# Optimization experiments

Measured on AMD Instinct MI355X. Metric: run time of the kernel, lower is better.

Reference implementation:

```python
import jax, jax.numpy as jnp
import numpy as np

B, S, D, H = 2, 2048, 1024, 16
DH = D // H


def setup_inputs() -> dict:
    key = jax.random.key(0)
    ks = jax.random.split(key, 9)
    s = 0.02
    return {
        "x": jax.random.normal(ks[0], (B, S, D), dtype=jnp.float32),
        "Wq": jax.random.normal(ks[1], (D, D), dtype=jnp.float32) * s,
        "bq": jnp.zeros((D,), dtype=jnp.float32),
        "Wk": jax.random.normal(ks[2], (D, D), dtype=jnp.float32) * s,
        "bk": jnp.zeros((D,), dtype=jnp.float32),
        "Wv": jax.random.normal(ks[3], (D, D), dtype=jnp.float32) * s,
        "bv": jnp.zeros((D,), dtype=jnp.float32),
        "Wo": jax.random.normal(ks[4], (D, D), dtype=jnp.float32) * s,
        "bo": jnp.zeros((D,), dtype=jnp.float32),
    }


def _split_heads(t):
    # [B,S,D] -> [B,H,S,Dh]
    return t.reshape(B, S, H, DH).transpose(0, 2, 1, 3)


def reference(x, Wq, bq, Wk, bk, Wv, bv, Wo, bo):
    q = _split_heads(x @ Wq + bq)
    k = _split_heads(x @ Wk + bk)
    v = _split_heads(x @ Wv + bv)
    scale = 1.0 / jnp.sqrt(jnp.float32(DH))
    # [B,H,S,S] attention scores (naive, materialized as in original)
    scores = jnp.einsum("bhqd,bhkd->bhqk", q, k) * scale
    probs = jax.nn.softmax(scores, axis=-1)
    attn = jnp.einsum("bhqk,bhkd->bhqd", probs, v)
    out = attn.transpose(0, 2, 1, 3).reshape(B, S, D)
    return out @ Wo + bo
```

## Files before the change

kernel.cpp:

```cpp
#include <hip/hip_runtime.h>
#include <math.h>

#define NB 2
#define NS 2048
#define ND 1024
#define NH 16
#define NDH 64
#define NM (NB * NS)
#define K2 (2 * ND)

typedef unsigned short ushortT;
typedef __attribute__((ext_vector_type(8))) short bf16x8;
typedef __attribute__((ext_vector_type(4))) float f32x4;
typedef __attribute__((ext_vector_type(16))) float f32x16;

__device__ inline unsigned short f2bf(float f) {
    union { float f; unsigned u; } v; v.f = f;
    unsigned r = v.u + 0x7FFFu + ((v.u >> 16) & 1u);
    return (unsigned short)(r >> 16);
}
__device__ inline float bf2f(unsigned short h) {
    union { unsigned u; float f; } v; v.u = ((unsigned)h) << 16; return v.f;
}
__device__ inline unsigned cvt_pk_bf16(float lo, float hi) {
    unsigned r;
    asm("v_cvt_pk_bf16_f32 %0, %1, %2" : "=v"(r) : "v"(lo), "v"(hi));
    return r;
}
__device__ inline void gl_lds16(const ushortT* g, ushortT* l) {
    __builtin_amdgcn_global_load_lds(
        (const __attribute__((address_space(1))) unsigned*)g,
        (__attribute__((address_space(3))) unsigned*)l, 16, 0, 0);
}

#define QSC 0.18033688011112042f

__global__ __launch_bounds__(256) void split_x(
    const float* __restrict__ x, ushortT* __restrict__ xh)
{
    int idx = (blockIdx.x * 256 + threadIdx.x) * 4;
    float4 v = *(const float4*)&x[idx];
    float fv[4] = {v.x, v.y, v.z, v.w};
    union { ushortT s[4]; uint2 u; } o;
#pragma unroll
    for (int j = 0; j < 4; ++j) o.s[j] = f2bf(fv[j]);
    *(uint2*)&xh[idx] = o.u;
}

__global__ __launch_bounds__(256) void split_w_t(
    const float* __restrict__ Wq, const float* __restrict__ Wk,
    const float* __restrict__ Wv, const float* __restrict__ Wo,
    ushortT* __restrict__ WtH, ushortT* __restrict__ WtO)
{
    const int z = blockIdx.z;
    const float* __restrict__ W = (z == 0) ? Wq : (z == 1) ? Wk : (z == 2) ? Wv : Wo;

    const int k0 = blockIdx.y * 64, n0 = blockIdx.x * 64;
    const int t = threadIdx.x;
    __shared__ float Ls[64][65];

#pragma unroll
    for (int i = 0; i < 4; ++i) {
        int kl = i * 16 + (t >> 4);
        int nl = (t & 15) << 2;
        float4 w4 = *(const float4*)&W[(size_t)(k0 + kl) * ND + n0 + nl];
        Ls[nl + 0][kl] = w4.x;
        Ls[nl + 1][kl] = w4.y;
        Ls[nl + 2][kl] = w4.z;
        Ls[nl + 3][kl] = w4.w;
    }
    __syncthreads();
#pragma unroll
    for (int i = 0; i < 16; ++i) {
        int flat = i * 256 + t;
        int n = flat >> 6, kk = flat & 63;
        float val = Ls[n][kk];
        unsigned short hi = f2bf(val);
        if (z < 3) {
            WtH[(size_t)z * ND * ND + (size_t)(n0 + n) * ND + (k0 + kk)] = hi;
        } else {
            WtO[(size_t)(n0 + n) * K2 + (k0 + kk)]      = hi;
            WtO[(size_t)(n0 + n) * K2 + ND + (k0 + kk)] = f2bf(val - bf2f(hi));
        }
    }
}

template <int OUTMODE>
__global__ __launch_bounds__(256) void gemm_split(
    const ushortT* __restrict__ A2,
    const ushortT* __restrict__ Wt,
    const float* __restrict__ b0, const float* __restrict__ b1, const float* __restrict__ b2,
    ushortT* __restrict__ Qo, ushortT* __restrict__ Ko, ushortT* __restrict__ Vtg,
    float* __restrict__ Ofp)
{
    const int z = blockIdx.z;
    const int AS = OUTMODE ? K2 : ND;
    const ushortT* __restrict__ Bt = OUTMODE ? Wt : Wt + (size_t)z * ND * ND;
    const float* __restrict__ bias = (z == 0) ? b0 : (z == 1) ? b1 : b2;

    const int L = blockIdx.y * 8 + blockIdx.x;
    const int rx = L & 7, q = L >> 3;
    const int m0 = (((q >> 3) << 3) + rx) * 128;
    const int n0 = (q & 7) * 128;

    const int tid = threadIdx.x;
    const int lane = tid & 63, w = tid >> 6;
    const int wrow = w >> 1, wcol = w & 1;
    const int a = lane & 15, g = lane >> 4;

    __shared__ __align__(16) ushortT Abuf[3][128 * 32];
    __shared__ __align__(16) ushortT Bbuf[3][128 * 32];

    f32x4 acc[4][4] = {};

    const int srow_l = tid >> 2;
    const int scc0 = tid & 3;
    const int swz = (a >> 1) & 3;

    const int nst = OUTMODE ? 96 : 32;

    auto stage = [&](int bufi, int ks) {
        const int kp = ks * 32;
        const int ac = OUTMODE ? ((kp < ND) ? kp : kp - ND) : kp;
        const int bc = OUTMODE ? ((kp < 2 * ND) ? kp : kp - 2 * ND) : kp;
#pragma unroll
        for (int t = 0; t < 2; ++t) {
            int r = t * 64 + srow_l;
            int sc = scc0 ^ ((r >> 1) & 3);
            gl_lds16(&A2[(size_t)(m0 + r) * AS + ac + (sc << 3)],
                     &Abuf[bufi][(t * 256 + w * 64) * 8]);
            gl_lds16(&Bt[(size_t)(n0 + r) * AS + bc + (sc << 3)],
                     &Bbuf[bufi][(t * 256 + w * 64) * 8]);
        }
    };

    stage(0, 0);
    stage(1, 1);
    int cur = 0;
    for (int i = 0; i < nst; ++i) {
        if (i + 1 < nst) {
            asm volatile("s_waitcnt vmcnt(4)" ::: "memory");
        } else {
            asm volatile("s_waitcnt vmcnt(0)" ::: "memory");
        }
        __builtin_amdgcn_s_barrier();

        if (i + 2 < nst) {
            int nb = cur + 2; if (nb >= 3) nb -= 3;
            stage(nb, i + 2);
        }

        bf16x8 af[4], bfr[4];
#pragma unroll
        for (int ii = 0; ii < 4; ++ii)
            af[ii] = *(const bf16x8*)&Abuf[cur][(wrow * 64 + ii * 16 + a) * 32 + ((g ^ swz) << 3)];
#pragma unroll
        for (int j = 0; j < 4; ++j)
            bfr[j] = *(const bf16x8*)&Bbuf[cur][(wcol * 64 + j * 16 + a) * 32 + ((g ^ swz) << 3)];
#pragma unroll
        for (int ii = 0; ii < 4; ++ii)
#pragma unroll
            for (int j = 0; j < 4; ++j)
                acc[ii][j] = __builtin_amdgcn_mfma_f32_16x16x32_bf16(af[ii], bfr[j], acc[ii][j], 0, 0, 0);

        ++cur; if (cur == 3) cur = 0;
    }

    float bj[4];
#pragma unroll
    for (int j = 0; j < 4; ++j) bj[j] = bias[n0 + wcol * 64 + j * 16 + a];

#pragma unroll
    for (int i = 0; i < 4; ++i) {
#pragma unroll
        for (int r = 0; r < 4; ++r) {
            int grow = m0 + wrow * 64 + i * 16 + g * 4 + r;
#pragma unroll
            for (int j = 0; j < 4; ++j) {
                int gcol = n0 + wcol * 64 + j * 16 + a;
                float v = acc[i][j][r] + bj[j];
                if (OUTMODE == 1) {
                    Ofp[(size_t)grow * ND + gcol] = v;
                } else {
                    int b = grow >> 11, s = grow & (NS - 1);
                    int h = gcol >> 6, dh = gcol & 63;
                    if (z == 0) {
                        Qo[((size_t)(b * NH + h) * NS + s) * NDH + dh] = f2bf(v * QSC);
                    } else if (z == 1) {
                        Ko[((size_t)(b * NH + h) * NS + s) * NDH + dh] = f2bf(v);
                    } else {
                        Vtg[((size_t)(b * NH + h) * NDH + dh) * NS + s] = f2bf(v);
                    }
                }
            }
        }
    }
}

__global__ __launch_bounds__(256) void attn_fwd2(
    const ushortT* __restrict__ Q, const ushortT* __restrict__ K,
    const ushortT* __restrict__ Vt, ushortT* __restrict__ A2o)
{
    const int bh = blockIdx.y;
    const int b = bh >> 4, h = bh & 15;
    const int q0 = blockIdx.x * 128;
    const int tid = threadIdx.x, lane = tid & 63, w = tid >> 6;
    const int ql = lane & 31;
    const int hi = lane >> 5;

    __shared__ __align__(16) unsigned smem4[8192];
    ushortT* sK = (ushortT*)smem4;
    ushortT* sV = sK + 2 * 4096;

    const ushortT* __restrict__ Kb  = K  + (size_t)bh * NS * NDH;
    const ushortT* __restrict__ Vtb = Vt + (size_t)bh * NDH * NS;

    bf16x8 qf[4];
    {
        const ushortT* qrow = Q + (size_t)bh * NS * NDH + (size_t)(q0 + w * 32 + ql) * NDH + hi * 8;
#pragma unroll
        for (int kc = 0; kc < 4; ++kc) qf[kc] = *(const bf16x8*)(qrow + kc * 16);
    }

    const int srw = lane >> 3;
    const int scc = lane & 7;

    float m_run = -INFINITY, l_run = 0.f;
    f32x16 oat[2] = {};

#pragma unroll
    for (int c = 0; c < 2; ++c) {
        int rK = c * 32 + w * 8 + srw;
        gl_lds16(&Kb[(size_t)rK * NDH + ((scc ^ srw) << 3)], &sK[(c * 256 + w * 64) * 8]);
        gl_lds16(&Vtb[(size_t)rK * NS + ((scc ^ srw) << 3)], &sV[(c * 256 + w * 64) * 8]);
    }

    for (int t = 0; t < NS / 64; ++t) {
        const int cur = t & 1;
        __syncthreads();
        if (t + 1 < NS / 64) {
            const int nxt = cur ^ 1;
            const int kv1 = (t + 1) * 64;
#pragma unroll
            for (int c = 0; c < 2; ++c) {
                int rK = c * 32 + w * 8 + srw;
                gl_lds16(&Kb[(size_t)(kv1 + rK) * NDH + ((scc ^ srw) << 3)],
                         &sK[(nxt * 4096) + (c * 256 + w * 64) * 8]);
                gl_lds16(&Vtb[(size_t)rK * NS + kv1 + ((scc ^ srw) << 3)],
                         &sV[(nxt * 4096) + (c * 256 + w * 64) * 8]);
            }
        }
        const ushortT* kbuf = sK + cur * 4096;
        const ushortT* vbuf = sV + cur * 4096;

        f32x16 st[2] = {};
#pragma unroll
        for (int s = 0; s < 2; ++s) {
            const int kv = s * 32 + ql;
#pragma unroll
            for (int kc = 0; kc < 4; ++kc) {
                bf16x8 kf = *(const bf16x8*)&kbuf[kv * 64 + (((kc * 2 + hi) ^ (ql & 7)) << 3)];
                st[s] = __builtin_amdgcn_mfma_f32_32x32x16_bf16(kf, qf[kc], st[s], 0, 0, 0);
            }
        }

        float mx = -INFINITY;
#pragma unroll
        for (int s = 0; s < 2; ++s)
#pragma unroll
            for (int r = 0; r < 16; ++r) mx = fmaxf(mx, st[s][r]);
        mx = fmaxf(mx, __shfl_xor(mx, 32));

        if (!__all(mx - m_run <= 8.0f)) {
            float mn = fmaxf(m_run, mx);
            float al = __builtin_amdgcn_exp2f(m_run - mn);
            m_run = mn;
            l_run *= al;
#pragma unroll
            for (int dt = 0; dt < 2; ++dt)
#pragma unroll
                for (int r = 0; r < 16; ++r) oat[dt][r] *= al;
        }
        float rs = 0.f;
#pragma unroll
        for (int s = 0; s < 2; ++s)
#pragma unroll
            for (int r = 0; r < 16; ++r) {
                float e = __builtin_amdgcn_exp2f(st[s][r] - m_run);
                st[s][r] = e;
                rs += e;
            }
        rs += __shfl_xor(rs, 32);
        l_run += rs;

#pragma unroll
        for (int ts = 0; ts < 4; ++ts) {
            const int s = ts >> 1, rb = 8 * (ts & 1);
            unsigned u0 = cvt_pk_bf16(st[s][rb + 0], st[s][rb + 1]);
            unsigned u1 = cvt_pk_bf16(st[s][rb + 2], st[s][rb + 3]);
            unsigned v0 = cvt_pk_bf16(st[s][rb + 4], st[s][rb + 5]);
            unsigned v1 = cvt_pk_bf16(st[s][rb + 6], st[s][rb + 7]);
            unsigned t0 = hi ? u0 : v0;
            unsigned t1 = hi ? u1 : v1;
            unsigned t0s = __shfl_xor(t0, 32);
            unsigned t1s = __shfl_xor(t1, 32);
            union { unsigned u[4]; bf16x8 v; } pf;
            pf.u[0] = hi ? t0s : u0;
            pf.u[1] = hi ? t1s : u1;
            pf.u[2] = hi ? v0 : t0s;
            pf.u[3] = hi ? v1 : t1s;
#pragma unroll
            for (int dt = 0; dt < 2; ++dt) {
                bf16x8 vf = *(const bf16x8*)&vbuf[(dt * 32 + ql) * 64 + (((ts * 2 + hi) ^ (ql & 7)) << 3)];
                oat[dt] = __builtin_amdgcn_mfma_f32_32x32x16_bf16(vf, pf.v, oat[dt], 0, 0, 0);
            }
        }
    }

    __syncthreads();
    unsigned* osc = smem4 + w * 2048;
    float inv = 1.0f / l_run;
#pragma unroll
    for (int dt = 0; dt < 2; ++dt)
#pragma unroll
        for (int r = 0; r < 16; ++r) {
            int d = dt * 32 + (r & 3) + 8 * (r >> 2) + 4 * hi;
            float o = oat[dt][r] * inv;
            unsigned short hb = f2bf(o);
            unsigned short lb = f2bf(o - bf2f(hb));
            osc[ql * 64 + (d ^ ql)] = (unsigned)hb | ((unsigned)lb << 16);
        }
    __syncthreads();
    const int qrd = lane >> 3;
    const int dbase = (lane & 7) * 8;
#pragma unroll
    for (int p = 0; p < 4; ++p) {
        int q = p * 8 + qrd;
        unsigned wv[8];
#pragma unroll
        for (int k = 0; k < 8; ++k)
            wv[k] = osc[q * 64 + ((dbase + k) ^ q)];
        union { ushortT s[8]; bf16x8 v; } hs, ls;
#pragma unroll
        for (int k = 0; k < 8; ++k) {
            hs.s[k] = (ushortT)(wv[k] & 0xffffu);
            ls.s[k] = (ushortT)(wv[k] >> 16);
        }
        size_t row = (size_t)(b * NS + q0 + w * 32 + q) * K2 + h * 64 + dbase;
        *(bf16x8*)&A2o[row]      = hs.v;
        *(bf16x8*)&A2o[row + ND] = ls.v;
    }
}

extern "C" void kernel_launch(void* const* d_in, const int* in_sizes, int n_in,
                              void* d_out, int out_size, void* d_ws, size_t ws_size,
                              hipStream_t stream)
{
    const float* x  = (const float*)d_in[0];
    const float* Wq = (const float*)d_in[1];
    const float* bq = (const float*)d_in[2];
    const float* Wk = (const float*)d_in[3];
    const float* bk = (const float*)d_in[4];
    const float* Wv = (const float*)d_in[5];
    const float* bv = (const float*)d_in[6];
    const float* Wo = (const float*)d_in[7];
    const float* bo = (const float*)d_in[8];
    float* out = (float*)d_out;

    ushortT* xh  = (ushortT*)d_ws;
    ushortT* WtH = xh  + (size_t)NM * ND;
    ushortT* WtO = WtH + (size_t)3 * ND * ND;
    ushortT* Qb  = WtO + (size_t)ND * K2;
    ushortT* Kb  = Qb  + (size_t)NM * ND;
    ushortT* Vtg = Kb  + (size_t)NM * ND;
    ushortT* A2  = Vtg + (size_t)NM * ND;

    split_x<<<dim3(NM * ND / 1024), 256, 0, stream>>>(x, xh);
    split_w_t<<<dim3(16, 16, 4), 256, 0, stream>>>(Wq, Wk, Wv, Wo, WtH, WtO);
    gemm_split<0><<<dim3(8, 32, 3), 256, 0, stream>>>(
        xh, WtH, bq, bk, bv, Qb, Kb, Vtg, nullptr);
    attn_fwd2<<<dim3(NS / 128, NB * NH), 256, 0, stream>>>(Qb, Kb, Vtg, A2);
    gemm_split<1><<<dim3(8, 32, 1), 256, 0, stream>>>(
        A2, WtO, bo, bo, bo, nullptr, nullptr, nullptr, out);
}
```

Measured before the change: 257.5 us.

## Split-K output GEMM with atomics, permute K rows to drop P shuffles

The output projection GEMM now splits its 96-step K loop across two z-slices. Each slice accumulates into an output that a new kernel pre-fills with the bias, using atomicAdd, so the grid doubles from 256 to 512 blocks. The attention kernel permutes which K row each lane loads, so the score accumulator layout matches the PV operand directly, removing the cross-half shuffles and selects. GEMM staging addresses are also precomputed once per thread. The float atomics make the summation order nondeterministic and add an extra launch plus a write pass over the output.

```diff
diff --git a/kernel.cpp b/kernel.cpp
--- a/kernel.cpp
+++ b/kernel.cpp
@@ -85,6 +85,16 @@
     }
 }
 
+__global__ __launch_bounds__(256) void out_init(
+    const float* __restrict__ bo, float* __restrict__ out)
+{
+    int idx = blockIdx.x * 256 + threadIdx.x;
+    int n4 = (idx & 255) << 2;
+    int m = idx >> 8;
+    float4 b4 = *(const float4*)&bo[n4];
+    *(float4*)&out[(size_t)m * ND + n4] = b4;
+}
+
 template <int OUTMODE>
 __global__ __launch_bounds__(256) void gemm_split(
     const ushortT* __restrict__ A2,
@@ -113,29 +123,29 @@
 
     f32x4 acc[4][4] = {};
 
-    const int srow_l = tid >> 2;
-    const int scc0 = tid & 3;
+    const int rS  = tid >> 2;
+    const int scS = (tid & 3) ^ ((rS >> 1) & 3);
+    const ushortT* pA0 = A2 + (size_t)(m0 + rS) * AS + (scS << 3);
+    const ushortT* pA1 = pA0 + (size_t)64 * AS;
+    const ushortT* pB0 = Bt + (size_t)(n0 + rS) * AS + (scS << 3);
+    const ushortT* pB1 = pB0 + (size_t)64 * AS;
+
     const int swz = (a >> 1) & 3;
-
-    const int nst = OUTMODE ? 96 : 32;
+    const int nst = OUTMODE ? 48 : 32;
+    const int ks0 = OUTMODE ? z * 48 : 0;
 
     auto stage = [&](int bufi, int ks) {
         const int kp = ks * 32;
-        const int ac = OUTMODE ? ((kp < ND) ? kp : kp - ND) : kp;
+        const int ac = (kp < ND) ? kp : kp - ND;
         const int bc = OUTMODE ? ((kp < 2 * ND) ? kp : kp - 2 * ND) : kp;
-#pragma unroll
-        for (int t = 0; t < 2; ++t) {
-            int r = t * 64 + srow_l;
-            int sc = scc0 ^ ((r >> 1) & 3);
-            gl_lds16(&A2[(size_t)(m0 + r) * AS + ac + (sc << 3)],
-                     &Abuf[bufi][(t * 256 + w * 64) * 8]);
-            gl_lds16(&Bt[(size_t)(n0 + r) * AS + bc + (sc << 3)],
-                     &Bbuf[bufi][(t * 256 + w * 64) * 8]);
-        }
+        gl_lds16(pA0 + ac, &Abuf[bufi][(w * 64) * 8]);
+        gl_lds16(pA1 + ac, &Abuf[bufi][(256 + w * 64) * 8]);
+        gl_lds16(pB0 + bc, &Bbuf[bufi][(w * 64) * 8]);
+        gl_lds16(pB1 + bc, &Bbuf[bufi][(256 + w * 64) * 8]);
     };
 
-    stage(0, 0);
-    stage(1, 1);
+    stage(0, ks0);
+    stage(1, ks0 + 1);
     int cur = 0;
     for (int i = 0; i < nst; ++i) {
         if (i + 1 < nst) {
@@ -147,7 +157,7 @@
 
         if (i + 2 < nst) {
             int nb = cur + 2; if (nb >= 3) nb -= 3;
-            stage(nb, i + 2);
+            stage(nb, ks0 + i + 2);
         }
 
         bf16x8 af[4], bfr[4];
@@ -167,8 +177,10 @@
     }
 
     float bj[4];
-#pragma unroll
-    for (int j = 0; j < 4; ++j) bj[j] = bias[n0 + wcol * 64 + j * 16 + a];
+    if (OUTMODE == 0) {
+#pragma unroll
+        for (int j = 0; j < 4; ++j) bj[j] = bias[n0 + wcol * 64 + j * 16 + a];
+    }
 
 #pragma unroll
     for (int i = 0; i < 4; ++i) {
@@ -178,10 +190,10 @@
 #pragma unroll
             for (int j = 0; j < 4; ++j) {
                 int gcol = n0 + wcol * 64 + j * 16 + a;
-                float v = acc[i][j][r] + bj[j];
                 if (OUTMODE == 1) {
-                    Ofp[(size_t)grow * ND + gcol] = v;
+                    atomicAdd(&Ofp[(size_t)grow * ND + gcol], acc[i][j][r]);
                 } else {
+                    float v = acc[i][j][r] + bj[j];
                     int b = grow >> 11, s = grow & (NS - 1);
                     int h = gcol >> 6, dh = gcol & 63;
                     if (z == 0) {
@@ -206,7 +218,11 @@
     const int q0 = blockIdx.x * 128;
     const int tid = threadIdx.x, lane = tid & 63, w = tid >> 6;
     const int ql = lane & 31;
-    const int hi = lane >> 5;
+    const int hb = lane >> 5;
+
+    const int prow = (((lane >> 3) & 1) << 4) | (((lane >> 2) & 1) << 3)
+                   | (((lane >> 4) & 1) << 2) | (lane & 3);
+    const int psw = prow & 7;
 
     __shared__ __align__(16) unsigned smem4[8192];
     ushortT* sK = (ushortT*)smem4;
@@ -217,7 +233,7 @@
 
     bf16x8 qf[4];
     {
-        const ushortT* qrow = Q + (size_t)bh * NS * NDH + (size_t)(q0 + w * 32 + ql) * NDH + hi * 8;
+        const ushortT* qrow = Q + (size_t)bh * NS * NDH + (size_t)(q0 + w * 32 + ql) * NDH + hb * 8;
 #pragma unroll
         for (int kc = 0; kc < 4; ++kc) qf[kc] = *(const bf16x8*)(qrow + kc * 16);
     }
@@ -256,10 +272,10 @@
         f32x16 st[2] = {};
 #pragma unroll
         for (int s = 0; s < 2; ++s) {
-            const int kv = s * 32 + ql;
+            const int kv = s * 32 + prow;
 #pragma unroll
             for (int kc = 0; kc < 4; ++kc) {
-                bf16x8 kf = *(const bf16x8*)&kbuf[kv * 64 + (((kc * 2 + hi) ^ (ql & 7)) << 3)];
+                bf16x8 kf = *(const bf16x8*)&kbuf[kv * 64 + (((kc * 2 + hb) ^ psw) << 3)];
                 st[s] = __builtin_amdgcn_mfma_f32_32x32x16_bf16(kf, qf[kc], st[s], 0, 0, 0);
             }
         }
@@ -295,23 +311,15 @@
 
 #pragma unroll
         for (int ts = 0; ts < 4; ++ts) {
-            const int s = ts >> 1, rb = 8 * (ts & 1);
-            unsigned u0 = cvt_pk_bf16(st[s][rb + 0], st[s][rb + 1]);
-            unsigned u1 = cvt_pk_bf16(st[s][rb + 2], st[s][rb + 3]);
-            unsigned v0 = cvt_pk_bf16(st[s][rb + 4], st[s][rb + 5]);
-            unsigned v1 = cvt_pk_bf16(st[s][rb + 6], st[s][rb + 7]);
-            unsigned t0 = hi ? u0 : v0;
-            unsigned t1 = hi ? u1 : v1;
-            unsigned t0s = __shfl_xor(t0, 32);
-            unsigned t1s = __shfl_xor(t1, 32);
+            const int s = ts >> 1, t4 = (ts & 1) * 4;
             union { unsigned u[4]; bf16x8 v; } pf;
-            pf.u[0] = hi ? t0s : u0;
-            pf.u[1] = hi ? t1s : u1;
-            pf.u[2] = hi ? v0 : t0s;
-            pf.u[3] = hi ? v1 : t1s;
+            pf.u[0] = cvt_pk_bf16(st[s][t4 + 0],  st[s][t4 + 1]);
+            pf.u[1] = cvt_pk_bf16(st[s][t4 + 2],  st[s][t4 + 3]);
+            pf.u[2] = cvt_pk_bf16(st[s][t4 + 8],  st[s][t4 + 9]);
+            pf.u[3] = cvt_pk_bf16(st[s][t4 + 10], st[s][t4 + 11]);
 #pragma unroll
             for (int dt = 0; dt < 2; ++dt) {
-                bf16x8 vf = *(const bf16x8*)&vbuf[(dt * 32 + ql) * 64 + (((ts * 2 + hi) ^ (ql & 7)) << 3)];
+                bf16x8 vf = *(const bf16x8*)&vbuf[(dt * 32 + ql) * 64 + (((ts * 2 + hb) ^ (ql & 7)) << 3)];
                 oat[dt] = __builtin_amdgcn_mfma_f32_32x32x16_bf16(vf, pf.v, oat[dt], 0, 0, 0);
             }
         }
@@ -324,29 +332,29 @@
     for (int dt = 0; dt < 2; ++dt)
 #pragma unroll
         for (int r = 0; r < 16; ++r) {
-            int d = dt * 32 + (r & 3) + 8 * (r >> 2) + 4 * hi;
+            int d = dt * 32 + (r & 3) + 8 * (r >> 2) + 4 * hb;
             float o = oat[dt][r] * inv;
-            unsigned short hb = f2bf(o);
-            unsigned short lb = f2bf(o - bf2f(hb));
-            osc[ql * 64 + (d ^ ql)] = (unsigned)hb | ((unsigned)lb << 16);
+            unsigned short hbx = f2bf(o);
+            unsigned short lbx = f2bf(o - bf2f(hbx));
+            osc[ql * 64 + (d ^ ql)] = (unsigned)hbx | ((unsigned)lbx << 16);
         }
     __syncthreads();
     const int qrd = lane >> 3;
     const int dbase = (lane & 7) * 8;
 #pragma unroll
     for (int p = 0; p < 4; ++p) {
-        int q = p * 8 + qrd;
+        int qq = p * 8 + qrd;
         unsigned wv[8];
 #pragma unroll
         for (int k = 0; k < 8; ++k)
-            wv[k] = osc[q * 64 + ((dbase + k) ^ q)];
+            wv[k] = osc[qq * 64 + ((dbase + k) ^ qq)];
         union { ushortT s[8]; bf16x8 v; } hs, ls;
 #pragma unroll
         for (int k = 0; k < 8; ++k) {
             hs.s[k] = (ushortT)(wv[k] & 0xffffu);
             ls.s[k] = (ushortT)(wv[k] >> 16);
         }
-        size_t row = (size_t)(b * NS + q0 + w * 32 + q) * K2 + h * 64 + dbase;
+        size_t row = (size_t)(b * NS + q0 + w * 32 + qq) * K2 + h * 64 + dbase;
         *(bf16x8*)&A2o[row]      = hs.v;
         *(bf16x8*)&A2o[row + ND] = ls.v;
     }
@@ -380,6 +388,7 @@
     gemm_split<0><<<dim3(8, 32, 3), 256, 0, stream>>>(
         xh, WtH, bq, bk, bv, Qb, Kb, Vtg, nullptr);
     attn_fwd2<<<dim3(NS / 128, NB * NH), 256, 0, stream>>>(Qb, Kb, Vtg, A2);
-    gemm_split<1><<<dim3(8, 32, 1), 256, 0, stream>>>(
+    out_init<<<dim3(NM * ND / 1024), 256, 0, stream>>>(bo, out);
+    gemm_split<1><<<dim3(8, 32, 2), 256, 0, stream>>>(
         A2, WtO, bo, bo, bo, nullptr, nullptr, nullptr, out);
 }
```

Measured after the change: 253.5 us. Within noise of the previous version (-1.5%).
